# Optimization experiments

Measured on AMD Instinct MI355X. Metric: run time of the kernel, lower is better.

## Reference

```python
import jax, jax.numpy as jnp
import numpy as np

THRESHOLD_SCALE = 0.75
EPS = 1e-6


def setup_inputs() -> dict:
    key = jax.random.key(0)
    k1, k2 = jax.random.split(key)
    B, IN, OUT = 8192, 4096, 4096
    x = jax.random.normal(k1, (B, IN), dtype=jnp.float32)
    # xavier_uniform-like init, then clip to [-1, 1] as clip_weights_ would
    bound = float(np.sqrt(6.0 / (IN + OUT)))
    weight = jax.random.uniform(k2, (OUT, IN), dtype=jnp.float32, minval=-bound, maxval=bound)
    bias = jnp.zeros((OUT,), dtype=jnp.float32)
    return {"x": x, "weight": weight, "bias": bias}


def reference(x, weight, bias):
    # per-output-row scale (detached in torch -> stop_gradient)
    scale = jax.lax.stop_gradient(
        jnp.maximum(jnp.mean(jnp.abs(weight), axis=1, keepdims=True), EPS)
    )  # [out, 1]
    threshold = scale * THRESHOLD_SCALE
    # ternary quantize: {-1, 0, +1}
    q = jnp.where(weight >= threshold, 1.0, jnp.where(weight <= -threshold, -1.0, 0.0)).astype(weight.dtype)
    # STE: forward = q, backward passes grad through where |w| <= 1
    mask = (jnp.abs(weight) <= 1.0).astype(weight.dtype)
    q_ste = weight * mask + jax.lax.stop_gradient(q - weight * mask)
    w_eff = q_ste * scale  # [out, in]
    return x @ w_eff.T + bias
```

## Files before the change

kernel.cpp:

```cpp
#include <hip/hip_runtime.h>
#include <hip/hip_bf16.h>

typedef __attribute__((ext_vector_type(4))) int i32x4;

#define GLOBAL_CAST(p) (const __attribute__((address_space(1))) void*)(p)
#define LDS_CAST(p)    (__attribute__((address_space(3))) void*)(p)

__global__ __launch_bounds__(256) void scale_quant_kernel(
    const float* __restrict__ w, float* __restrict__ scale,
    signed char* __restrict__ q, int K)
{
    const int row = blockIdx.x;
    const int tid = threadIdx.x;
    const float* wrow = w + (size_t)row * K;

    float s = 0.f;
    const int nvec = K >> 2;
    const float4* wv = (const float4*)wrow;
    for (int i = tid; i < nvec; i += blockDim.x) {
        float4 v = wv[i];
        s += fabsf(v.x) + fabsf(v.y) + fabsf(v.z) + fabsf(v.w);
    }
    #pragma unroll
    for (int off = 32; off > 0; off >>= 1) s += __shfl_down(s, off);

    __shared__ float red[4];
    const int lane = tid & 63, wid = tid >> 6;
    if (lane == 0) red[wid] = s;
    __syncthreads();
    const float total = red[0] + red[1] + red[2] + red[3];
    const float sc = fmaxf(total / (float)K, 1e-6f);
    const float thr = sc * 0.75f;
    if (tid == 0) scale[row] = sc;

    if (q != nullptr) {
        char4* qv = (char4*)(q + (size_t)row * K);
        for (int i = tid; i < nvec; i += blockDim.x) {
            float4 v = wv[i];
            char4 o;
            o.x = (v.x >= thr) ? 1 : ((v.x <= -thr) ? -1 : 0);
            o.y = (v.y >= thr) ? 1 : ((v.y <= -thr) ? -1 : 0);
            o.z = (v.z >= thr) ? 1 : ((v.z <= -thr) ? -1 : 0);
            o.w = (v.w >= thr) ? 1 : ((v.w <= -thr) ? -1 : 0);
            qv[i] = o;
        }
    }
}

__global__ __launch_bounds__(256) void x_quant_kernel(
    const float* __restrict__ x, float* __restrict__ sx,
    signed char* __restrict__ xq, int K)
{
    const int row = blockIdx.x;
    const int tid = threadIdx.x;
    const float4* xv = (const float4*)(x + (size_t)row * K);
    const int nvec = K >> 2;

    float am = 0.f;
    for (int i = tid; i < nvec; i += blockDim.x) {
        float4 v = xv[i];
        am = fmaxf(am, fmaxf(fmaxf(fabsf(v.x), fabsf(v.y)), fmaxf(fabsf(v.z), fabsf(v.w))));
    }
    #pragma unroll
    for (int off = 32; off > 0; off >>= 1) am = fmaxf(am, __shfl_down(am, off));

    __shared__ float red[4];
    const int lane = tid & 63, wid = tid >> 6;
    if (lane == 0) red[wid] = am;
    __syncthreads();
    const float amax = fmaxf(fmaxf(red[0], red[1]), fmaxf(red[2], red[3]));
    const float inv = (amax > 0.f) ? (127.f / amax) : 0.f;
    if (tid == 0) sx[row] = amax * (1.f / 127.f);

    char4* qv = (char4*)(xq + (size_t)row * K);
    for (int i = tid; i < nvec; i += blockDim.x) {
        float4 v = xv[i];
        char4 o;
        o.x = (signed char)__float2int_rn(v.x * inv);
        o.y = (signed char)__float2int_rn(v.y * inv);
        o.z = (signed char)__float2int_rn(v.z * inv);
        o.w = (signed char)__float2int_rn(v.w * inv);
        qv[i] = o;
    }
}

#define BM 256
#define BN 256
#define BK 128

__global__ __launch_bounds__(512, 2) void gemm256_i8_kernel(
    const signed char* __restrict__ Xq,
    const signed char* __restrict__ Qq,
    const float* __restrict__ sx,
    const float* __restrict__ scale,
    const float* __restrict__ bias,
    float* __restrict__ out, int M, int N, int K)
{
    __shared__ __align__(16) char lds[131072];

    const int tid  = threadIdx.x;
    const int lane = tid & 63;
    const int wid  = tid >> 6;
    const int wm   = wid >> 2;
    const int wn   = wid & 3;
    const int kh   = lane >> 4;
    const int lr   = lane & 15;

    int bid = blockIdx.x;
    const int nwg = gridDim.x;
    if ((nwg & 7) == 0) { const int cpx = nwg >> 3; bid = (bid & 7) * cpx + (bid >> 3); }
    const int nbn = N / BN;
    const int tm = bid / nbn, tn = bid % nbn;
    const int arow0 = tm * BM;
    const int brow0 = tn * BN;
    const int NT = K / BK;

    unsigned aoff[2][4], boff[2][2];
    #pragma unroll
    for (int ks = 0; ks < 2; ++ks) {
        const int c = kh + ks * 4;
        #pragma unroll
        for (int mf = 0; mf < 4; ++mf) {
            const int row = wm * 128 + mf * 16 + lr;
            aoff[ks][mf] = (unsigned)(row * 128 + ((c ^ (row & 7)) << 4));
        }
        #pragma unroll
        for (int nf = 0; nf < 2; ++nf) {
            const int row = wn * 64 + nf * 16 + lr;
            boff[ks][nf] = (unsigned)(32768 + row * 128 + ((c ^ (row & 7)) << 4));
        }
    }

    const int r0 = tid >> 3;
    const int c0 = (((tid & 7) ^ (r0 & 7)) << 4);
    const int ci1 = 512 + tid;
    const int r1 = ci1 >> 3;
    const int c1 = (((ci1 & 7) ^ (r1 & 7)) << 4);

    const signed char* asrc[2][2];
    const signed char* bsrc[2][2];
    unsigned adst[2][2], bdst[2][2];
    #pragma unroll
    for (int hh = 0; hh < 2; ++hh) {
        asrc[hh][0] = Xq + (size_t)(arow0 + hh * 128 + r0) * K + BK + c0;
        asrc[hh][1] = Xq + (size_t)(arow0 + hh * 128 + r1) * K + BK + c1;
        bsrc[hh][0] = Qq + (size_t)(brow0 + hh * 128 + r0) * K + BK + c0;
        bsrc[hh][1] = Qq + (size_t)(brow0 + hh * 128 + r1) * K + BK + c1;
        adst[hh][0] = (unsigned)(hh * 16384 + tid * 16);
        adst[hh][1] = (unsigned)(hh * 16384 + ci1 * 16);
        bdst[hh][0] = (unsigned)(32768 + hh * 16384 + tid * 16);
        bdst[hh][1] = (unsigned)(32768 + hh * 16384 + ci1 * 16);
    }

    #pragma unroll
    for (int hh = 0; hh < 2; ++hh) {
        const int rowA = arow0 + hh * 128, rowB = brow0 + hh * 128;
        const signed char* ga0 = Xq + (size_t)(rowA + r0) * K + c0;
        const signed char* ga1 = Xq + (size_t)(rowA + r1) * K + c1;
        const signed char* gb0 = Qq + (size_t)(rowB + r0) * K + c0;
        const signed char* gb1 = Qq + (size_t)(rowB + r1) * K + c1;
        __builtin_amdgcn_global_load_lds(GLOBAL_CAST(ga0), LDS_CAST(lds + adst[hh][0]), 16, 0, 0);
        __builtin_amdgcn_global_load_lds(GLOBAL_CAST(ga1), LDS_CAST(lds + adst[hh][1]), 16, 0, 0);
        __builtin_amdgcn_global_load_lds(GLOBAL_CAST(gb0), LDS_CAST(lds + bdst[hh][0]), 16, 0, 0);
        __builtin_amdgcn_global_load_lds(GLOBAL_CAST(gb1), LDS_CAST(lds + bdst[hh][1]), 16, 0, 0);
    }
    asm volatile("s_waitcnt vmcnt(0)" ::: "memory");
    __builtin_amdgcn_sched_barrier(0);
    __builtin_amdgcn_s_barrier();

    i32x4 acc[8][4] = {};
    i32x4 a[2][4];
    i32x4 b0[2][2], b1[2][2];

    #define RDA(ks, mf, EX) (*(const i32x4*)(lds + (tb | aoff[ks][mf]) + (EX)))
    #define RDB(ks, nf, EX) (*(const i32x4*)(lds + (tb | boff[ks][nf]) + (EX)))
    #define MFMA16(AR, BR, AI, BJ)                                            \
        _Pragma("unroll")                                                     \
        for (int ks = 0; ks < 2; ++ks)                                        \
            _Pragma("unroll")                                                 \
            for (int mf = 0; mf < 4; ++mf)                                    \
                _Pragma("unroll")                                             \
                for (int nf = 0; nf < 2; ++nf)                                \
                    acc[(AI) + mf][(BJ) + nf] =                               \
                        __builtin_amdgcn_mfma_i32_16x16x64_i8(                \
                            AR[ks][mf], BR[ks][nf], acc[(AI) + mf][(BJ) + nf], 0, 0, 0);

    for (int t = 0; t < NT; ++t) {
        const unsigned tb = (unsigned)(t & 1) << 16;
        const unsigned ta = tb ^ 0x10000u;
        const bool doS = (t < NT - 1);

        if (doS) {
            #pragma unroll
            for (int hh = 0; hh < 2; ++hh) {
                __builtin_amdgcn_global_load_lds(GLOBAL_CAST(asrc[hh][0]), LDS_CAST(lds + (ta | adst[hh][0])), 16, 0, 0);
                __builtin_amdgcn_global_load_lds(GLOBAL_CAST(asrc[hh][1]), LDS_CAST(lds + (ta | adst[hh][1])), 16, 0, 0);
                __builtin_amdgcn_global_load_lds(GLOBAL_CAST(bsrc[hh][0]), LDS_CAST(lds + (ta | bdst[hh][0])), 16, 0, 0);
                __builtin_amdgcn_global_load_lds(GLOBAL_CAST(bsrc[hh][1]), LDS_CAST(lds + (ta | bdst[hh][1])), 16, 0, 0);
            }
        }

        #pragma unroll
        for (int ks = 0; ks < 2; ++ks) {
            #pragma unroll
            for (int nf = 0; nf < 2; ++nf) b0[ks][nf] = RDB(ks, nf, 0);
            #pragma unroll
            for (int nf = 0; nf < 2; ++nf) b1[ks][nf] = RDB(ks, nf, 4096);
            #pragma unroll
            for (int mf = 0; mf < 4; ++mf) a[ks][mf] = RDA(ks, mf, 0);
        }
        __builtin_amdgcn_s_setprio(1);
        MFMA16(a, b0, 0, 0)
        MFMA16(a, b1, 0, 2)
        __builtin_amdgcn_s_setprio(0);

        #pragma unroll
        for (int ks = 0; ks < 2; ++ks)
            #pragma unroll
            for (int mf = 0; mf < 4; ++mf) a[ks][mf] = RDA(ks, mf, 8192);
        __builtin_amdgcn_s_setprio(1);
        MFMA16(a, b1, 4, 2)
        MFMA16(a, b0, 4, 0)
        __builtin_amdgcn_s_setprio(0);

        #pragma unroll
        for (int hh = 0; hh < 2; ++hh) {
            asrc[hh][0] += BK; asrc[hh][1] += BK;
            bsrc[hh][0] += BK; bsrc[hh][1] += BK;
        }
        asm volatile("s_waitcnt vmcnt(0)" ::: "memory");
        __builtin_amdgcn_sched_barrier(0);
        __builtin_amdgcn_s_barrier();
    }
    #undef RDA
    #undef RDB
    #undef MFMA16

    float sxv[32];
    #pragma unroll
    for (int mf = 0; mf < 8; ++mf)
        #pragma unroll
        for (int r = 0; r < 4; ++r)
            sxv[mf * 4 + r] = sx[arow0 + wm * 128 + mf * 16 + kh * 4 + r];

    #pragma unroll
    for (int nf = 0; nf < 4; ++nf) {
        const int gn = brow0 + wn * 64 + nf * 16 + lr;
        const float sc = scale[gn];
        const float bs = bias[gn];
        #pragma unroll
        for (int mf = 0; mf < 8; ++mf) {
            const size_t gm = (size_t)arow0 + wm * 128 + mf * 16 + kh * 4;
            #pragma unroll
            for (int r = 0; r < 4; ++r)
                out[(gm + r) * (size_t)N + gn] =
                    (float)acc[mf][nf][r] * (sxv[mf * 4 + r] * sc) + bs;
        }
    }
}

__global__ __launch_bounds__(256) void fb_gemm_kernel(
    const float* __restrict__ X, const float* __restrict__ W,
    const float* __restrict__ scale, const float* __restrict__ bias,
    float* __restrict__ out, int M, int N, int K)
{
    __shared__ float xs[16][16];
    __shared__ float qs[16][17];
    const int tx = threadIdx.x & 15, ty = threadIdx.x >> 4;
    const int m = blockIdx.y * 16 + ty;
    const int n = blockIdx.x * 16 + tx;
    const int nrow = blockIdx.x * 16 + ty;
    const int mL = min(m, M - 1);
    const int nrowL = min(nrow, N - 1);
    const float thr = scale[nrowL] * 0.75f;
    float acc = 0.f;
    for (int k0 = 0; k0 < K; k0 += 16) {
        xs[ty][tx] = X[(size_t)mL * K + k0 + tx];
        const float w = W[(size_t)nrowL * K + k0 + tx];
        qs[ty][tx] = (w >= thr) ? 1.f : ((w <= -thr) ? -1.f : 0.f);
        __syncthreads();
        #pragma unroll
        for (int kk = 0; kk < 16; ++kk) acc += xs[ty][kk] * qs[tx][kk];
        __syncthreads();
    }
    if (m < M && n < N) out[(size_t)m * N + n] = scale[n] * acc + bias[n];
}

extern "C" void kernel_launch(void* const* d_in, const int* in_sizes, int n_in,
                              void* d_out, int out_size, void* d_ws, size_t ws_size,
                              hipStream_t stream)
{
    const float* x    = (const float*)d_in[0];
    const float* w    = (const float*)d_in[1];
    const float* bias = (const float*)d_in[2];
    float* out = (float*)d_out;

    const int N = in_sizes[2];
    const int K = in_sizes[1] / N;
    const int M = in_sizes[0] / K;

    const size_t scOff = 0;
    const size_t sxOff = (scOff + (size_t)N * 4 + 255) & ~(size_t)255;
    const size_t qOff  = (sxOff + (size_t)M * 4 + 255) & ~(size_t)255;
    const size_t xqOff = (qOff + (size_t)N * K + 255) & ~(size_t)255;
    const size_t need  = xqOff + (size_t)M * K;

    float* scale = (float*)((char*)d_ws + scOff);

    const bool fast = (ws_size >= need) &&
                      (M % BM == 0) && (N % BN == 0) && (K % BK == 0) &&
                      ((K & 3) == 0) && (K / BK >= 4) &&
                      (((M / BM) * (N / BN)) % 8 == 0);

    if (fast) {
        float* sx        = (float*)((char*)d_ws + sxOff);
        signed char* q   = (signed char*)((char*)d_ws + qOff);
        signed char* xq  = (signed char*)((char*)d_ws + xqOff);

        scale_quant_kernel<<<N, 256, 0, stream>>>(w, scale, q, K);
        x_quant_kernel<<<M, 256, 0, stream>>>(x, sx, xq, K);

        const int grid = (M / BM) * (N / BN);
        gemm256_i8_kernel<<<grid, 512, 0, stream>>>(xq, q, sx, scale, bias, out, M, N, K);
    } else {
        scale_quant_kernel<<<N, 256, 0, stream>>>(w, scale, nullptr, K);
        dim3 g((N + 15) / 16, (M + 15) / 16);
        fb_gemm_kernel<<<g, 256, 0, stream>>>(x, w, scale, bias, out, M, N, K);
    }
}
```

Before: 194.6 us.

## Shrink int8 GEMM tile to 128x128 with 256 threads and staggered loads

Replaces the 256x256-tile, 512-thread int8 MFMA GEMM with a 128x128-tile, 256-thread version that uses 64KB of LDS. The aim is more workgroups per CU and more latency hiding. The B-tile prefetch now issues after the first MFMA half, with an extra workgroup barrier, so global loads are spread across the iteration. Smaller tiles cut data reuse per tile and raise L2 and global traffic. The extra barrier adds synchronization cost.

```diff
diff --git a/kernel.cpp b/kernel.cpp
--- a/kernel.cpp
+++ b/kernel.cpp
@@ -84,11 +84,11 @@
     }
 }
 
-#define BM 256
-#define BN 256
+#define BM 128
+#define BN 128
 #define BK 128
 
-__global__ __launch_bounds__(512, 2) void gemm256_i8_kernel(
+__global__ __launch_bounds__(256, 2) void gemm128_i8_kernel(
     const signed char* __restrict__ Xq,
     const signed char* __restrict__ Qq,
     const float* __restrict__ sx,
@@ -96,13 +96,13 @@
     const float* __restrict__ bias,
     float* __restrict__ out, int M, int N, int K)
 {
-    __shared__ __align__(16) char lds[131072];
+    __shared__ __align__(16) char lds[65536];
 
     const int tid  = threadIdx.x;
     const int lane = tid & 63;
     const int wid  = tid >> 6;
-    const int wm   = wid >> 2;
-    const int wn   = wid & 3;
+    const int wm   = wid >> 1;
+    const int wn   = wid & 1;
     const int kh   = lane >> 4;
     const int lr   = lane & 15;
 
@@ -115,133 +115,123 @@
     const int brow0 = tn * BN;
     const int NT = K / BK;
 
-    unsigned aoff[2][4], boff[2][2];
+    unsigned aoff[2][4], boff[2][4];
     #pragma unroll
     for (int ks = 0; ks < 2; ++ks) {
         const int c = kh + ks * 4;
         #pragma unroll
         for (int mf = 0; mf < 4; ++mf) {
-            const int row = wm * 128 + mf * 16 + lr;
+            const int row = wm * 64 + mf * 16 + lr;
             aoff[ks][mf] = (unsigned)(row * 128 + ((c ^ (row & 7)) << 4));
         }
         #pragma unroll
-        for (int nf = 0; nf < 2; ++nf) {
+        for (int nf = 0; nf < 4; ++nf) {
             const int row = wn * 64 + nf * 16 + lr;
-            boff[ks][nf] = (unsigned)(32768 + row * 128 + ((c ^ (row & 7)) << 4));
-        }
-    }
-
-    const int r0 = tid >> 3;
-    const int c0 = (((tid & 7) ^ (r0 & 7)) << 4);
-    const int ci1 = 512 + tid;
-    const int r1 = ci1 >> 3;
-    const int c1 = (((ci1 & 7) ^ (r1 & 7)) << 4);
-
-    const signed char* asrc[2][2];
-    const signed char* bsrc[2][2];
-    unsigned adst[2][2], bdst[2][2];
-    #pragma unroll
-    for (int hh = 0; hh < 2; ++hh) {
-        asrc[hh][0] = Xq + (size_t)(arow0 + hh * 128 + r0) * K + BK + c0;
-        asrc[hh][1] = Xq + (size_t)(arow0 + hh * 128 + r1) * K + BK + c1;
-        bsrc[hh][0] = Qq + (size_t)(brow0 + hh * 128 + r0) * K + BK + c0;
-        bsrc[hh][1] = Qq + (size_t)(brow0 + hh * 128 + r1) * K + BK + c1;
-        adst[hh][0] = (unsigned)(hh * 16384 + tid * 16);
-        adst[hh][1] = (unsigned)(hh * 16384 + ci1 * 16);
-        bdst[hh][0] = (unsigned)(32768 + hh * 16384 + tid * 16);
-        bdst[hh][1] = (unsigned)(32768 + hh * 16384 + ci1 * 16);
-    }
-
-    #pragma unroll
-    for (int hh = 0; hh < 2; ++hh) {
-        const int rowA = arow0 + hh * 128, rowB = brow0 + hh * 128;
-        const signed char* ga0 = Xq + (size_t)(rowA + r0) * K + c0;
-        const signed char* ga1 = Xq + (size_t)(rowA + r1) * K + c1;
-        const signed char* gb0 = Qq + (size_t)(rowB + r0) * K + c0;
-        const signed char* gb1 = Qq + (size_t)(rowB + r1) * K + c1;
-        __builtin_amdgcn_global_load_lds(GLOBAL_CAST(ga0), LDS_CAST(lds + adst[hh][0]), 16, 0, 0);
-        __builtin_amdgcn_global_load_lds(GLOBAL_CAST(ga1), LDS_CAST(lds + adst[hh][1]), 16, 0, 0);
-        __builtin_amdgcn_global_load_lds(GLOBAL_CAST(gb0), LDS_CAST(lds + bdst[hh][0]), 16, 0, 0);
-        __builtin_amdgcn_global_load_lds(GLOBAL_CAST(gb1), LDS_CAST(lds + bdst[hh][1]), 16, 0, 0);
+            boff[ks][nf] = (unsigned)(0x4000 + row * 128 + ((c ^ (row & 7)) << 4));
+        }
+    }
+
+    int rj[4]; unsigned dstj[4]; int cj[4];
+    #pragma unroll
+    for (int j = 0; j < 4; ++j) {
+        const int ci = tid + j * 256;
+        rj[j] = ci >> 3;
+        cj[j] = (((ci & 7) ^ (rj[j] & 7)) << 4);
+        dstj[j] = (unsigned)(ci * 16);
+    }
+
+    const signed char* asrc[4];
+    const signed char* bsrc[4];
+    #pragma unroll
+    for (int j = 0; j < 4; ++j) {
+        asrc[j] = Xq + (size_t)(arow0 + rj[j]) * K + BK + cj[j];
+        bsrc[j] = Qq + (size_t)(brow0 + rj[j]) * K + BK + cj[j];
+    }
+
+    #pragma unroll
+    for (int j = 0; j < 4; ++j) {
+        const signed char* ga = Xq + (size_t)(arow0 + rj[j]) * K + cj[j];
+        const signed char* gb = Qq + (size_t)(brow0 + rj[j]) * K + cj[j];
+        __builtin_amdgcn_global_load_lds(GLOBAL_CAST(ga), LDS_CAST(lds + dstj[j]), 16, 0, 0);
+        __builtin_amdgcn_global_load_lds(GLOBAL_CAST(gb), LDS_CAST(lds + (dstj[j] | 0x4000u)), 16, 0, 0);
     }
     asm volatile("s_waitcnt vmcnt(0)" ::: "memory");
     __builtin_amdgcn_sched_barrier(0);
     __builtin_amdgcn_s_barrier();
 
-    i32x4 acc[8][4] = {};
-    i32x4 a[2][4];
-    i32x4 b0[2][2], b1[2][2];
-
-    #define RDA(ks, mf, EX) (*(const i32x4*)(lds + (tb | aoff[ks][mf]) + (EX)))
-    #define RDB(ks, nf, EX) (*(const i32x4*)(lds + (tb | boff[ks][nf]) + (EX)))
-    #define MFMA16(AR, BR, AI, BJ)                                            \
+    i32x4 acc[4][4] = {};
+    i32x4 a[2][2];
+    i32x4 b[2][4];
+
+    #define RDA(ks, mf) (*(const i32x4*)(lds + (tb | aoff[ks][mf])))
+    #define RDB(ks, nf) (*(const i32x4*)(lds + (tb | boff[ks][nf])))
+    #define MFMA8(AI, BJ)                                                     \
         _Pragma("unroll")                                                     \
         for (int ks = 0; ks < 2; ++ks)                                        \
             _Pragma("unroll")                                                 \
-            for (int mf = 0; mf < 4; ++mf)                                    \
+            for (int mh = 0; mh < 2; ++mh)                                    \
                 _Pragma("unroll")                                             \
-                for (int nf = 0; nf < 2; ++nf)                                \
-                    acc[(AI) + mf][(BJ) + nf] =                               \
+                for (int nh = 0; nh < 2; ++nh)                                \
+                    acc[(AI) + mh][(BJ) + nh] =                               \
                         __builtin_amdgcn_mfma_i32_16x16x64_i8(                \
-                            AR[ks][mf], BR[ks][nf], acc[(AI) + mf][(BJ) + nf], 0, 0, 0);
+                            a[ks][mh], b[ks][(BJ) + nh],                      \
+                            acc[(AI) + mh][(BJ) + nh], 0, 0, 0);
 
     for (int t = 0; t < NT; ++t) {
-        const unsigned tb = (unsigned)(t & 1) << 16;
-        const unsigned ta = tb ^ 0x10000u;
+        const unsigned tb = (unsigned)(t & 1) << 15;
+        const unsigned ta = tb ^ 0x8000u;
         const bool doS = (t < NT - 1);
 
         if (doS) {
             #pragma unroll
-            for (int hh = 0; hh < 2; ++hh) {
-                __builtin_amdgcn_global_load_lds(GLOBAL_CAST(asrc[hh][0]), LDS_CAST(lds + (ta | adst[hh][0])), 16, 0, 0);
-                __builtin_amdgcn_global_load_lds(GLOBAL_CAST(asrc[hh][1]), LDS_CAST(lds + (ta | adst[hh][1])), 16, 0, 0);
-                __builtin_amdgcn_global_load_lds(GLOBAL_CAST(bsrc[hh][0]), LDS_CAST(lds + (ta | bdst[hh][0])), 16, 0, 0);
-                __builtin_amdgcn_global_load_lds(GLOBAL_CAST(bsrc[hh][1]), LDS_CAST(lds + (ta | bdst[hh][1])), 16, 0, 0);
-            }
-        }
-
+            for (int j = 0; j < 4; ++j)
+                __builtin_amdgcn_global_load_lds(GLOBAL_CAST(asrc[j]), LDS_CAST(lds + (ta | dstj[j])), 16, 0, 0);
+        }
         #pragma unroll
         for (int ks = 0; ks < 2; ++ks) {
             #pragma unroll
-            for (int nf = 0; nf < 2; ++nf) b0[ks][nf] = RDB(ks, nf, 0);
-            #pragma unroll
-            for (int nf = 0; nf < 2; ++nf) b1[ks][nf] = RDB(ks, nf, 4096);
-            #pragma unroll
-            for (int mf = 0; mf < 4; ++mf) a[ks][mf] = RDA(ks, mf, 0);
+            for (int nf = 0; nf < 4; ++nf) b[ks][nf] = RDB(ks, nf);
+            #pragma unroll
+            for (int mh = 0; mh < 2; ++mh) a[ks][mh] = RDA(ks, mh);
         }
         __builtin_amdgcn_s_setprio(1);
-        MFMA16(a, b0, 0, 0)
-        MFMA16(a, b1, 0, 2)
+        MFMA8(0, 0)
+        MFMA8(0, 2)
         __builtin_amdgcn_s_setprio(0);
 
+        if (doS) {
+            #pragma unroll
+            for (int j = 0; j < 4; ++j)
+                __builtin_amdgcn_global_load_lds(GLOBAL_CAST(bsrc[j]), LDS_CAST(lds + (ta | dstj[j] | 0x4000u)), 16, 0, 0);
+        }
+        __builtin_amdgcn_s_barrier();
+
         #pragma unroll
         for (int ks = 0; ks < 2; ++ks)
             #pragma unroll
-            for (int mf = 0; mf < 4; ++mf) a[ks][mf] = RDA(ks, mf, 8192);
+            for (int mh = 0; mh < 2; ++mh) a[ks][mh] = RDA(ks, 2 + mh);
         __builtin_amdgcn_s_setprio(1);
-        MFMA16(a, b1, 4, 2)
-        MFMA16(a, b0, 4, 0)
+        MFMA8(2, 2)
+        MFMA8(2, 0)
         __builtin_amdgcn_s_setprio(0);
 
         #pragma unroll
-        for (int hh = 0; hh < 2; ++hh) {
-            asrc[hh][0] += BK; asrc[hh][1] += BK;
-            bsrc[hh][0] += BK; bsrc[hh][1] += BK;
-        }
+        for (int j = 0; j < 4; ++j) { asrc[j] += BK; bsrc[j] += BK; }
+
         asm volatile("s_waitcnt vmcnt(0)" ::: "memory");
         __builtin_amdgcn_sched_barrier(0);
         __builtin_amdgcn_s_barrier();
     }
     #undef RDA
     #undef RDB
-    #undef MFMA16
-
-    float sxv[32];
-    #pragma unroll
-    for (int mf = 0; mf < 8; ++mf)
+    #undef MFMA8
+
+    float sxv[16];
+    #pragma unroll
+    for (int mf = 0; mf < 4; ++mf)
         #pragma unroll
         for (int r = 0; r < 4; ++r)
-            sxv[mf * 4 + r] = sx[arow0 + wm * 128 + mf * 16 + kh * 4 + r];
+            sxv[mf * 4 + r] = sx[arow0 + wm * 64 + mf * 16 + kh * 4 + r];
 
     #pragma unroll
     for (int nf = 0; nf < 4; ++nf) {
@@ -249,8 +239,8 @@
         const float sc = scale[gn];
         const float bs = bias[gn];
         #pragma unroll
-        for (int mf = 0; mf < 8; ++mf) {
-            const size_t gm = (size_t)arow0 + wm * 128 + mf * 16 + kh * 4;
+        for (int mf = 0; mf < 4; ++mf) {
+            const size_t gm = (size_t)arow0 + wm * 64 + mf * 16 + kh * 4;
             #pragma unroll
             for (int r = 0; r < 4; ++r)
                 out[(gm + r) * (size_t)N + gn] =
@@ -309,7 +299,7 @@
 
     const bool fast = (ws_size >= need) &&
                       (M % BM == 0) && (N % BN == 0) && (K % BK == 0) &&
-                      ((K & 3) == 0) && (K / BK >= 4) &&
+                      ((K & 3) == 0) && (K / BK >= 2) &&
                       (((M / BM) * (N / BN)) % 8 == 0);
 
     if (fast) {
@@ -321,7 +311,7 @@
         x_quant_kernel<<<M, 256, 0, stream>>>(x, sx, xq, K);
 
         const int grid = (M / BM) * (N / BN);
-        gemm256_i8_kernel<<<grid, 512, 0, stream>>>(xq, q, sx, scale, bias, out, M, N, K);
+        gemm128_i8_kernel<<<grid, 256, 0, stream>>>(xq, q, sx, scale, bias, out, M, N, K);
     } else {
         scale_quant_kernel<<<N, 256, 0, stream>>>(w, scale, nullptr, K);
         dim3 g((N + 15) / 16, (M + 15) / 16);
```

After: 205.1 us. 1.05x slower.

## Restructure int8 GEMM mainloop into two k-phases with staggered prefetch, register-cache quant rows

Applied to the files above, without the earlier changes.

The GEMM inner loop now works in two k-half phases per tile. Each phase loads all 8 A and 4 B fragments, and the two warp-row groups start on opposite k-halves (an XOR on the k offset) to spread LDS bank traffic. The global-to-LDS prefetch of A is issued before the first phase and B before the second, so the async copies are spread across compute. The quantization kernels also gain a K=4096 fast path that holds the row in registers instead of reading it from memory a second time. This adds register pressure (a[8], b[4]) and may change MFMA/LDS interleaving.

```diff
diff --git a/kernel.cpp b/kernel.cpp
--- a/kernel.cpp
+++ b/kernel.cpp
@@ -13,26 +13,56 @@
     const int row = blockIdx.x;
     const int tid = threadIdx.x;
     const float* wrow = w + (size_t)row * K;
-
-    float s = 0.f;
     const int nvec = K >> 2;
     const float4* wv = (const float4*)wrow;
+
+    __shared__ float red[4];
+    const int lane = tid & 63, wid = tid >> 6;
+
+    if (nvec == 1024) {
+        float4 v[4];
+        float s = 0.f;
+        #pragma unroll
+        for (int j = 0; j < 4; ++j) {
+            v[j] = wv[tid + j * 256];
+            s += fabsf(v[j].x) + fabsf(v[j].y) + fabsf(v[j].z) + fabsf(v[j].w);
+        }
+        #pragma unroll
+        for (int off = 32; off > 0; off >>= 1) s += __shfl_down(s, off);
+        if (lane == 0) red[wid] = s;
+        __syncthreads();
+        const float total = red[0] + red[1] + red[2] + red[3];
+        const float sc = fmaxf(total / (float)K, 1e-6f);
+        const float thr = sc * 0.75f;
+        if (tid == 0) scale[row] = sc;
+        if (q != nullptr) {
+            char4* qv = (char4*)(q + (size_t)row * K);
+            #pragma unroll
+            for (int j = 0; j < 4; ++j) {
+                char4 o;
+                o.x = (v[j].x >= thr) ? 1 : ((v[j].x <= -thr) ? -1 : 0);
+                o.y = (v[j].y >= thr) ? 1 : ((v[j].y <= -thr) ? -1 : 0);
+                o.z = (v[j].z >= thr) ? 1 : ((v[j].z <= -thr) ? -1 : 0);
+                o.w = (v[j].w >= thr) ? 1 : ((v[j].w <= -thr) ? -1 : 0);
+                qv[tid + j * 256] = o;
+            }
+        }
+        return;
+    }
+
+    float s = 0.f;
     for (int i = tid; i < nvec; i += blockDim.x) {
         float4 v = wv[i];
         s += fabsf(v.x) + fabsf(v.y) + fabsf(v.z) + fabsf(v.w);
     }
     #pragma unroll
     for (int off = 32; off > 0; off >>= 1) s += __shfl_down(s, off);
-
-    __shared__ float red[4];
-    const int lane = tid & 63, wid = tid >> 6;
     if (lane == 0) red[wid] = s;
     __syncthreads();
     const float total = red[0] + red[1] + red[2] + red[3];
     const float sc = fmaxf(total / (float)K, 1e-6f);
     const float thr = sc * 0.75f;
     if (tid == 0) scale[row] = sc;
-
     if (q != nullptr) {
         char4* qv = (char4*)(q + (size_t)row * K);
         for (int i = tid; i < nvec; i += blockDim.x) {
@@ -56,6 +86,38 @@
     const float4* xv = (const float4*)(x + (size_t)row * K);
     const int nvec = K >> 2;
 
+    __shared__ float red[4];
+    const int lane = tid & 63, wid = tid >> 6;
+
+    if (nvec == 1024) {
+        float4 v[4];
+        float am = 0.f;
+        #pragma unroll
+        for (int j = 0; j < 4; ++j) {
+            v[j] = xv[tid + j * 256];
+            am = fmaxf(am, fmaxf(fmaxf(fabsf(v[j].x), fabsf(v[j].y)),
+                                 fmaxf(fabsf(v[j].z), fabsf(v[j].w))));
+        }
+        #pragma unroll
+        for (int off = 32; off > 0; off >>= 1) am = fmaxf(am, __shfl_down(am, off));
+        if (lane == 0) red[wid] = am;
+        __syncthreads();
+        const float amax = fmaxf(fmaxf(red[0], red[1]), fmaxf(red[2], red[3]));
+        const float inv = (amax > 0.f) ? (127.f / amax) : 0.f;
+        if (tid == 0) sx[row] = amax * (1.f / 127.f);
+        char4* qv = (char4*)(xq + (size_t)row * K);
+        #pragma unroll
+        for (int j = 0; j < 4; ++j) {
+            char4 o;
+            o.x = (signed char)__float2int_rn(v[j].x * inv);
+            o.y = (signed char)__float2int_rn(v[j].y * inv);
+            o.z = (signed char)__float2int_rn(v[j].z * inv);
+            o.w = (signed char)__float2int_rn(v[j].w * inv);
+            qv[tid + j * 256] = o;
+        }
+        return;
+    }
+
     float am = 0.f;
     for (int i = tid; i < nvec; i += blockDim.x) {
         float4 v = xv[i];
@@ -63,15 +125,11 @@
     }
     #pragma unroll
     for (int off = 32; off > 0; off >>= 1) am = fmaxf(am, __shfl_down(am, off));
-
-    __shared__ float red[4];
-    const int lane = tid & 63, wid = tid >> 6;
     if (lane == 0) red[wid] = am;
     __syncthreads();
     const float amax = fmaxf(fmaxf(red[0], red[1]), fmaxf(red[2], red[3]));
     const float inv = (amax > 0.f) ? (127.f / amax) : 0.f;
     if (tid == 0) sx[row] = amax * (1.f / 127.f);
-
     char4* qv = (char4*)(xq + (size_t)row * K);
     for (int i = tid; i < nvec; i += blockDim.x) {
         float4 v = xv[i];
@@ -105,6 +163,7 @@
     const int wn   = wid & 3;
     const int kh   = lane >> 4;
     const int lr   = lane & 15;
+    const int grp  = wm;
 
     int bid = blockIdx.x;
     const int nwg = gridDim.x;
@@ -115,20 +174,16 @@
     const int brow0 = tn * BN;
     const int NT = K / BK;
 
-    unsigned aoff[2][4], boff[2][2];
-    #pragma unroll
-    for (int ks = 0; ks < 2; ++ks) {
-        const int c = kh + ks * 4;
-        #pragma unroll
-        for (int mf = 0; mf < 4; ++mf) {
-            const int row = wm * 128 + mf * 16 + lr;
-            aoff[ks][mf] = (unsigned)(row * 128 + ((c ^ (row & 7)) << 4));
-        }
-        #pragma unroll
-        for (int nf = 0; nf < 2; ++nf) {
-            const int row = wn * 64 + nf * 16 + lr;
-            boff[ks][nf] = (unsigned)(32768 + row * 128 + ((c ^ (row & 7)) << 4));
-        }
+    unsigned aoff[8], boff[4];
+    #pragma unroll
+    for (int mf = 0; mf < 8; ++mf) {
+        const int row = wm * 128 + mf * 16 + lr;
+        aoff[mf] = (unsigned)(row * 128 + ((kh ^ (row & 7)) << 4));
+    }
+    #pragma unroll
+    for (int nf = 0; nf < 4; ++nf) {
+        const int row = wn * 64 + nf * 16 + lr;
+        boff[nf] = (unsigned)(32768 + row * 128 + ((kh ^ (row & 7)) << 4));
     }
 
     const int r0 = tid >> 3;
@@ -169,21 +224,26 @@
     __builtin_amdgcn_s_barrier();
 
     i32x4 acc[8][4] = {};
-    i32x4 a[2][4];
-    i32x4 b0[2][2], b1[2][2];
-
-    #define RDA(ks, mf, EX) (*(const i32x4*)(lds + (tb | aoff[ks][mf]) + (EX)))
-    #define RDB(ks, nf, EX) (*(const i32x4*)(lds + (tb | boff[ks][nf]) + (EX)))
-    #define MFMA16(AR, BR, AI, BJ)                                            \
-        _Pragma("unroll")                                                     \
-        for (int ks = 0; ks < 2; ++ks)                                        \
-            _Pragma("unroll")                                                 \
-            for (int mf = 0; mf < 4; ++mf)                                    \
-                _Pragma("unroll")                                             \
-                for (int nf = 0; nf < 2; ++nf)                                \
-                    acc[(AI) + mf][(BJ) + nf] =                               \
-                        __builtin_amdgcn_mfma_i32_16x16x64_i8(                \
-                            AR[ks][mf], BR[ks][nf], acc[(AI) + mf][(BJ) + nf], 0, 0, 0);
+    i32x4 a[8], b[4];
+
+    #define PHASE(KX)                                                          \
+        _Pragma("unroll")                                                      \
+        for (int nf = 0; nf < 4; ++nf)                                         \
+            b[nf] = *(const i32x4*)(lds + ((tb | boff[nf]) ^ (KX)));           \
+        _Pragma("unroll")                                                      \
+        for (int mf = 0; mf < 8; ++mf)                                         \
+            a[mf] = *(const i32x4*)(lds + ((tb | aoff[mf]) ^ (KX)));           \
+        __builtin_amdgcn_s_setprio(1);                                         \
+        _Pragma("unroll")                                                      \
+        for (int mf = 0; mf < 8; ++mf)                                         \
+            _Pragma("unroll")                                                  \
+            for (int nf = 0; nf < 4; ++nf)                                     \
+                acc[mf][nf] = __builtin_amdgcn_mfma_i32_16x16x64_i8(           \
+                    a[mf], b[nf], acc[mf][nf], 0, 0, 0);                       \
+        __builtin_amdgcn_s_setprio(0);
+
+    const unsigned kx0 = (unsigned)grp << 6;
+    const unsigned kx1 = kx0 ^ 64u;
 
     for (int t = 0; t < NT; ++t) {
         const unsigned tb = (unsigned)(t & 1) << 16;
@@ -195,33 +255,18 @@
             for (int hh = 0; hh < 2; ++hh) {
                 __builtin_amdgcn_global_load_lds(GLOBAL_CAST(asrc[hh][0]), LDS_CAST(lds + (ta | adst[hh][0])), 16, 0, 0);
                 __builtin_amdgcn_global_load_lds(GLOBAL_CAST(asrc[hh][1]), LDS_CAST(lds + (ta | adst[hh][1])), 16, 0, 0);
+            }
+        }
+        PHASE(kx0)
+
+        if (doS) {
+            #pragma unroll
+            for (int hh = 0; hh < 2; ++hh) {
                 __builtin_amdgcn_global_load_lds(GLOBAL_CAST(bsrc[hh][0]), LDS_CAST(lds + (ta | bdst[hh][0])), 16, 0, 0);
                 __builtin_amdgcn_global_load_lds(GLOBAL_CAST(bsrc[hh][1]), LDS_CAST(lds + (ta | bdst[hh][1])), 16, 0, 0);
             }
         }
-
-        #pragma unroll
-        for (int ks = 0; ks < 2; ++ks) {
-            #pragma unroll
-            for (int nf = 0; nf < 2; ++nf) b0[ks][nf] = RDB(ks, nf, 0);
-            #pragma unroll
-            for (int nf = 0; nf < 2; ++nf) b1[ks][nf] = RDB(ks, nf, 4096);
-            #pragma unroll
-            for (int mf = 0; mf < 4; ++mf) a[ks][mf] = RDA(ks, mf, 0);
-        }
-        __builtin_amdgcn_s_setprio(1);
-        MFMA16(a, b0, 0, 0)
-        MFMA16(a, b1, 0, 2)
-        __builtin_amdgcn_s_setprio(0);
-
-        #pragma unroll
-        for (int ks = 0; ks < 2; ++ks)
-            #pragma unroll
-            for (int mf = 0; mf < 4; ++mf) a[ks][mf] = RDA(ks, mf, 8192);
-        __builtin_amdgcn_s_setprio(1);
-        MFMA16(a, b1, 4, 2)
-        MFMA16(a, b0, 4, 0)
-        __builtin_amdgcn_s_setprio(0);
+        PHASE(kx1)
 
         #pragma unroll
         for (int hh = 0; hh < 2; ++hh) {
@@ -232,9 +277,7 @@
         __builtin_amdgcn_sched_barrier(0);
         __builtin_amdgcn_s_barrier();
     }
-    #undef RDA
-    #undef RDB
-    #undef MFMA16
+    #undef PHASE
 
     float sxv[32];
     #pragma unroll
```

After: 180.4 us (median of 2 runs). 7.3% less time.
